# Kernel optimization log

Hardware: AMD Instinct MI355X
Metric: run time of the kernel (lower is better)

## Reference

```python
import jax, jax.numpy as jnp
import numpy as np


def setup_inputs() -> dict:
    key = jax.random.key(0)
    k1, k2, k3 = jax.random.split(key, 3)
    B, L, D, K = 4, 4096, 2048, 4
    x = jax.random.normal(k1, (B, L, D), dtype=jnp.float32)
    # depthwise kernel, channel-last layout (K, 1, D); torch weight is (D,1,K) = w.transpose(2,1,0)
    w = jax.random.normal(k2, (K, 1, D), dtype=jnp.float32) * 0.1
    b = jax.random.normal(k3, (D,), dtype=jnp.float32) * 0.1
    return {"x": x, "w": w, "b": b}


def reference(x, w, b):
    """Depthwise causal conv1d, channel-last.
    x: (B, L, D); w: (K, 1, D); b: (D,). Returns (B, L, D).
    Matches torch: Conv1d(D, D, K, groups=D, padding=K-1)(x.T)[..., :L].T
    which is exactly a causal conv (left pad K-1, trim to L).
    """
    K = w.shape[0]
    D = x.shape[-1]
    y = jax.lax.conv_general_dilated(
        x, w,
        window_strides=(1,),
        padding=[(K - 1, 0)],  # causal: left pad only
        feature_group_count=D,
        dimension_numbers=("NWC", "WIO", "NWC"),
    )
    return y + b
```

## Files before the change

kernel.cpp:

```cpp
#include <hip/hip_runtime.h>


#define CONV_B 4
#define CONV_L 4096
#define CONV_D 2048
#define CONV_K 4
#define CONV_T 8
#define CONV_D4 (CONV_D / 4)
#define CONV_LC (CONV_L / CONV_T)

typedef float nfloat4 __attribute__((ext_vector_type(4)));

__global__ __launch_bounds__(256) void short_conv_kernel(
    const float* __restrict__ x,
    const float* __restrict__ w,
    const float* __restrict__ bias,
    float* __restrict__ y)
{
    const int gid = blockIdx.x * blockDim.x + threadIdx.x;
    const int d4 = gid % CONV_D4;
    const int rest = gid / CONV_D4;
    const int lchunk = rest % CONV_LC;
    const int b = rest / CONV_LC;
    const int l0 = lchunk * CONV_T;
    const int d = d4 * 4;

    const float4* __restrict__ x4 =
        (const float4*)(x + (size_t)b * CONV_L * CONV_D) + d4;
    float4* __restrict__ y4 =
        (float4*)(y + (size_t)b * CONV_L * CONV_D) + d4;

    const float4 zero = make_float4(0.f, 0.f, 0.f, 0.f);

    float4 xc[CONV_T];
#pragma unroll
    for (int t = 0; t < CONV_T; ++t) {
        xc[t] = x4[(size_t)(l0 + t) * CONV_D4];
    }
    float4 xm3 = (l0 >= 3) ? x4[(size_t)(l0 - 3) * CONV_D4] : zero;
    float4 xm2 = (l0 >= 2) ? x4[(size_t)(l0 - 2) * CONV_D4] : zero;
    float4 xm1 = (l0 >= 1) ? x4[(size_t)(l0 - 1) * CONV_D4] : zero;

    const float4 w0 = *(const float4*)(w + 0 * CONV_D + d);
    const float4 w1 = *(const float4*)(w + 1 * CONV_D + d);
    const float4 w2 = *(const float4*)(w + 2 * CONV_D + d);
    const float4 w3 = *(const float4*)(w + 3 * CONV_D + d);
    const float4 bv = *(const float4*)(bias + d);

#pragma unroll
    for (int t = 0; t < CONV_T; ++t) {
        const float4 a3 = xm3, a2 = xm2, a1 = xm1, a0 = xc[t];
        nfloat4 r;
        r.x = fmaf(w0.x, a3.x, fmaf(w1.x, a2.x, fmaf(w2.x, a1.x, fmaf(w3.x, a0.x, bv.x))));
        r.y = fmaf(w0.y, a3.y, fmaf(w1.y, a2.y, fmaf(w2.y, a1.y, fmaf(w3.y, a0.y, bv.y))));
        r.z = fmaf(w0.z, a3.z, fmaf(w1.z, a2.z, fmaf(w2.z, a1.z, fmaf(w3.z, a0.z, bv.z))));
        r.w = fmaf(w0.w, a3.w, fmaf(w1.w, a2.w, fmaf(w2.w, a1.w, fmaf(w3.w, a0.w, bv.w))));

        __builtin_nontemporal_store(r, (nfloat4*)&y4[(size_t)(l0 + t) * CONV_D4]);

        xm3 = xm2;
        xm2 = xm1;
        xm1 = a0;
    }
}

extern "C" void kernel_launch(void* const* d_in, const int* in_sizes, int n_in,
                              void* d_out, int out_size, void* d_ws, size_t ws_size,
                              hipStream_t stream) {
    const float* x = (const float*)d_in[0];
    const float* w = (const float*)d_in[1];
    const float* b = (const float*)d_in[2];
    float* y = (float*)d_out;

    const int total_threads = CONV_B * CONV_LC * CONV_D4;
    const int block = 256;
    const int grid = total_threads / block;

    short_conv_kernel<<<grid, block, 0, stream>>>(x, w, b, y);
}
```

Before: 231.5 us.

## Stage input tiles with halo in LDS via direct global-to-LDS loads

Each block now loads a 35-row by 256-channel tile (32 output rows plus a 3-row causal halo) into shared memory using direct global-to-LDS loads, then each wave computes 8 output rows from LDS. This cuts redundant halo re-reads from global memory compared with the per-thread 8-row chunks. It adds LDS usage and a block barrier, which may limit occupancy, and depends on 16-byte direct LDS load support.

After: 230.5 us. Within noise of the previous version (-0.5%).

```diff
diff --git a/kernel.cpp b/kernel.cpp
--- a/kernel.cpp
+++ b/kernel.cpp
@@ -1,13 +1,17 @@
 #include <hip/hip_runtime.h>
+#include <stdint.h>
 
 
-#define CONV_B 4
-#define CONV_L 4096
-#define CONV_D 2048
-#define CONV_K 4
-#define CONV_T 8
-#define CONV_D4 (CONV_D / 4)
-#define CONV_LC (CONV_L / CONV_T)
+#define CB 4
+#define CL 4096
+#define CD 2048
+#define STRIP 256
+#define SF4 (STRIP / 4)
+#define ROWS 32
+#define HALO 3
+#define LROWS (ROWS + HALO)
+#define NSTRIP (CD / STRIP)
+#define NCHUNK (CL / ROWS)
 
 typedef float nfloat4 __attribute__((ext_vector_type(4)));
 
@@ -17,46 +21,66 @@
     const float* __restrict__ bias,
     float* __restrict__ y)
 {
-    const int gid = blockIdx.x * blockDim.x + threadIdx.x;
-    const int d4 = gid % CONV_D4;
-    const int rest = gid / CONV_D4;
-    const int lchunk = rest % CONV_LC;
-    const int b = rest / CONV_LC;
-    const int l0 = lchunk * CONV_T;
-    const int d = d4 * 4;
+    __shared__ float lds[LROWS * STRIP];
 
-    const float4* __restrict__ x4 =
-        (const float4*)(x + (size_t)b * CONV_L * CONV_D) + d4;
-    float4* __restrict__ y4 =
-        (float4*)(y + (size_t)b * CONV_L * CONV_D) + d4;
+    const int tid  = threadIdx.x;
+    const int lane = tid & 63;
+    const int wv   = tid >> 6;
 
-    const float4 zero = make_float4(0.f, 0.f, 0.f, 0.f);
+    const int bid    = blockIdx.x;
+    const int strip  = bid & (NSTRIP - 1);
+    const int lchunk = (bid >> 3) & (NCHUNK - 1);
+    const int b      = bid >> 10;
 
-    float4 xc[CONV_T];
-#pragma unroll
-    for (int t = 0; t < CONV_T; ++t) {
-        xc[t] = x4[(size_t)(l0 + t) * CONV_D4];
+    const int l0 = lchunk * ROWS;
+    const int c0 = strip * STRIP;
+
+    const float* xs = x + (size_t)b * CL * CD + c0;
+    float*       ys = y + (size_t)b * CL * CD + c0;
+
+    if (l0 == 0 && tid < HALO * SF4) {
+        ((float4*)lds)[tid] = make_float4(0.f, 0.f, 0.f, 0.f);
     }
-    float4 xm3 = (l0 >= 3) ? x4[(size_t)(l0 - 3) * CONV_D4] : zero;
-    float4 xm2 = (l0 >= 2) ? x4[(size_t)(l0 - 2) * CONV_D4] : zero;
-    float4 xm1 = (l0 >= 1) ? x4[(size_t)(l0 - 1) * CONV_D4] : zero;
 
-    const float4 w0 = *(const float4*)(w + 0 * CONV_D + d);
-    const float4 w1 = *(const float4*)(w + 1 * CONV_D + d);
-    const float4 w2 = *(const float4*)(w + 2 * CONV_D + d);
-    const float4 w3 = *(const float4*)(w + 3 * CONV_D + d);
-    const float4 bv = *(const float4*)(bias + d);
+    for (int r = wv; r < LROWS; r += 4) {
+        const int l = l0 - HALO + r;
+        if (l >= 0) {
+            const float* gsrc = xs + (size_t)l * CD + lane * 4;
+            float* ldst = &lds[r * STRIP + lane * 4];
+            __builtin_amdgcn_global_load_lds(
+                (const __attribute__((address_space(1))) uint32_t*)gsrc,
+                (__attribute__((address_space(3))) uint32_t*)ldst,
+                16, 0, 0);
+        }
+    }
+
+    const float4 w0 = *(const float4*)(w + 0 * CD + c0 + lane * 4);
+    const float4 w1 = *(const float4*)(w + 1 * CD + c0 + lane * 4);
+    const float4 w2 = *(const float4*)(w + 2 * CD + c0 + lane * 4);
+    const float4 w3 = *(const float4*)(w + 3 * CD + c0 + lane * 4);
+    const float4 bv = *(const float4*)(bias + c0 + lane * 4);
+
+    __syncthreads();
+
+    const int o0 = wv * 8;
+    const float4* lrow = (const float4*)lds + lane;
+
+    float4 xm3 = lrow[(o0 + 0) * SF4];
+    float4 xm2 = lrow[(o0 + 1) * SF4];
+    float4 xm1 = lrow[(o0 + 2) * SF4];
 
 #pragma unroll
-    for (int t = 0; t < CONV_T; ++t) {
-        const float4 a3 = xm3, a2 = xm2, a1 = xm1, a0 = xc[t];
+    for (int t = 0; t < 8; ++t) {
+        const float4 a0 = lrow[(o0 + t + HALO) * SF4];
+
         nfloat4 r;
-        r.x = fmaf(w0.x, a3.x, fmaf(w1.x, a2.x, fmaf(w2.x, a1.x, fmaf(w3.x, a0.x, bv.x))));
-        r.y = fmaf(w0.y, a3.y, fmaf(w1.y, a2.y, fmaf(w2.y, a1.y, fmaf(w3.y, a0.y, bv.y))));
-        r.z = fmaf(w0.z, a3.z, fmaf(w1.z, a2.z, fmaf(w2.z, a1.z, fmaf(w3.z, a0.z, bv.z))));
-        r.w = fmaf(w0.w, a3.w, fmaf(w1.w, a2.w, fmaf(w2.w, a1.w, fmaf(w3.w, a0.w, bv.w))));
+        r.x = fmaf(w0.x, xm3.x, fmaf(w1.x, xm2.x, fmaf(w2.x, xm1.x, fmaf(w3.x, a0.x, bv.x))));
+        r.y = fmaf(w0.y, xm3.y, fmaf(w1.y, xm2.y, fmaf(w2.y, xm1.y, fmaf(w3.y, a0.y, bv.y))));
+        r.z = fmaf(w0.z, xm3.z, fmaf(w1.z, xm2.z, fmaf(w2.z, xm1.z, fmaf(w3.z, a0.z, bv.z))));
+        r.w = fmaf(w0.w, xm3.w, fmaf(w1.w, xm2.w, fmaf(w2.w, xm1.w, fmaf(w3.w, a0.w, bv.w))));
 
-        __builtin_nontemporal_store(r, (nfloat4*)&y4[(size_t)(l0 + t) * CONV_D4]);
+        const int l = l0 + o0 + t;
+        __builtin_nontemporal_store(r, (nfloat4*)(ys + (size_t)l * CD + lane * 4));
 
         xm3 = xm2;
         xm2 = xm1;
@@ -72,9 +96,6 @@
     const float* b = (const float*)d_in[2];
     float* y = (float*)d_out;
 
-    const int total_threads = CONV_B * CONV_LC * CONV_D4;
-    const int block = 256;
-    const int grid = total_threads / block;
-
-    short_conv_kernel<<<grid, block, 0, stream>>>(x, w, b, y);
+    const int grid = CB * NCHUNK * NSTRIP;
+    short_conv_kernel<<<grid, 256, 0, stream>>>(x, w, b, y);
 }
```
